# Kernel optimization log

Measured on AMD Instinct MI355X. Metric: run time of the kernel, lower is better.

## Reference

```python
import jax, jax.numpy as jnp
import numpy as np

HEAD_DIM = 32
KERNEL = 3
DILATION = 2


def _unfold(x, k, dil):
    """torch.nn.Unfold with stride=1, padding=dil*(k-1)//2.
    x: [B, C, H, W] -> patches [B, C, k*k, H, W] (kernel positions row-major,
    channel-major overall, matching torch's (B, C*k*k, L) layout)."""
    B, C, H, W = x.shape
    pad = dil * (k - 1) // 2
    xp = jnp.pad(x, ((0, 0), (0, 0), (pad, pad), (pad, pad)))
    patches = jnp.stack(
        [xp[:, :, i * dil:i * dil + H, j * dil:j * dil + W]
         for i in range(k) for j in range(k)],
        axis=2,
    )
    return patches  # [B, C, k*k, H, W]


def setup_inputs() -> dict:
    key = jax.random.key(0)
    kq, kk, kv = jax.random.split(key, 3)
    shape = (8, 384, 56, 56)
    return {
        "q": jax.random.normal(kq, shape, dtype=jnp.float32),
        "k": jax.random.normal(kk, shape, dtype=jnp.float32),
        "v": jax.random.normal(kv, shape, dtype=jnp.float32),
    }


def reference(q, k, v):
    B, d, H, W = q.shape
    h = d // HEAD_DIM
    N = H * W
    k2 = KERNEL * KERNEL
    scale = HEAD_DIM ** (-0.5)

    # q: [B, h, N, hd]
    qr = q.reshape(B, h, HEAD_DIM, N).transpose(0, 1, 3, 2)
    # k patches: [B, h, hd, k2, N]
    kp = _unfold(k, KERNEL, DILATION).reshape(B, h, HEAD_DIM, k2, N)
    attn = jnp.einsum('bhnd,bhdkn->bhnk', qr, kp) * scale
    attn = jax.nn.softmax(attn, axis=-1)
    # v patches: [B, h, hd, k2, N]
    vp = _unfold(v, KERNEL, DILATION).reshape(B, h, HEAD_DIM, k2, N)
    out = jnp.einsum('bhnk,bhdkn->bhnd', attn, vp)  # [B, h, N, hd]
    # transpose(1,2) then reshape(B, H, W, d)
    return out.transpose(0, 2, 1, 3).reshape(B, H, W, d)
```

## Files before the change

kernel.cpp:

```cpp
#include <hip/hip_runtime.h>

#define HD 32
#define NHEADS 12
#define HH 56
#define WW 56
#define NN (HH * WW)
#define BB 8
#define CC (HD * NHEADS)

__global__ __launch_bounds__(256) void dilate_attn_kernel(
    const float* __restrict__ q,
    const float* __restrict__ k,
    const float* __restrict__ v,
    float* __restrict__ out)
{
    const int n = blockIdx.x * blockDim.x + threadIdx.x;
    if (n >= NN) return;
    const int bh = blockIdx.y;
    const int b = bh / NHEADS;
    const int head = bh - b * NHEADS;
    const int y = n / WW;
    const int x = n - y * WW;

    const size_t base = ((size_t)b * CC + (size_t)head * HD) * NN;
    const float* qb = q + base + n;

    float qv[HD];
#pragma unroll
    for (int d = 0; d < HD; ++d) qv[d] = qb[(size_t)d * NN];

    float lg[9];
#pragma unroll
    for (int kk = 0; kk < 9; ++kk) {
        const int dy = ((kk / 3) - 1) * 2;
        const int dx = ((kk % 3) - 1) * 2;
        const int ny = y + dy;
        const int nx = x + dx;
        float s = 0.f;
        if ((unsigned)ny < HH && (unsigned)nx < WW) {
            const float* kb = k + base + (size_t)(ny * WW + nx);
#pragma unroll
            for (int d = 0; d < HD; ++d) s = fmaf(qv[d], kb[(size_t)d * NN], s);
        }
        lg[kk] = s * 0.17677669529663689f;
    }

    float m = lg[0];
#pragma unroll
    for (int kk = 1; kk < 9; ++kk) m = fmaxf(m, lg[kk]);
    float wsum = 0.f;
#pragma unroll
    for (int kk = 0; kk < 9; ++kk) { lg[kk] = __expf(lg[kk] - m); wsum += lg[kk]; }
    const float inv = 1.f / wsum;

    float acc[HD];
#pragma unroll
    for (int d = 0; d < HD; ++d) acc[d] = 0.f;
#pragma unroll
    for (int kk = 0; kk < 9; ++kk) {
        const int dy = ((kk / 3) - 1) * 2;
        const int dx = ((kk % 3) - 1) * 2;
        const int ny = y + dy;
        const int nx = x + dx;
        if ((unsigned)ny < HH && (unsigned)nx < WW) {
            const float w = lg[kk] * inv;
            const float* vb = v + base + (size_t)(ny * WW + nx);
#pragma unroll
            for (int d = 0; d < HD; ++d) acc[d] = fmaf(w, vb[(size_t)d * NN], acc[d]);
        }
    }

    float* ob = out + (((size_t)b * HH + y) * WW + x) * CC + (size_t)head * HD;
#pragma unroll
    for (int d = 0; d < HD; d += 4) {
        float4 val = make_float4(acc[d], acc[d + 1], acc[d + 2], acc[d + 3]);
        *reinterpret_cast<float4*>(ob + d) = val;
    }
}

extern "C" void kernel_launch(void* const* d_in, const int* in_sizes, int n_in,
                              void* d_out, int out_size, void* d_ws, size_t ws_size,
                              hipStream_t stream) {
    const float* q = (const float*)d_in[0];
    const float* k = (const float*)d_in[1];
    const float* v = (const float*)d_in[2];
    float* out = (float*)d_out;

    dim3 block(256);
    dim3 grid((NN + 255) / 256, BB * NHEADS);
    dilate_attn_kernel<<<grid, block, 0, stream>>>(q, k, v, out);
}
```

Measured before the change: 188.8 us.

## Split head dimension across two thread halves with shared-memory logit reduction

Result: no change. 185.2 us (-1.9%).

```diff
diff --git a/kernel.cpp b/kernel.cpp
--- a/kernel.cpp
+++ b/kernel.cpp
@@ -1,12 +1,15 @@
 #include <hip/hip_runtime.h>
 
 #define HD 32
+#define HALF 16
 #define NHEADS 12
 #define HH 56
 #define WW 56
 #define NN (HH * WW)
 #define BB 8
 #define CC (HD * NHEADS)
+#define TILE_N 128
+#define SCALE 0.17677669529663689f
 
 __global__ __launch_bounds__(256) void dilate_attn_kernel(
     const float* __restrict__ q,
@@ -14,67 +17,85 @@
     const float* __restrict__ v,
     float* __restrict__ out)
 {
-    const int n = blockIdx.x * blockDim.x + threadIdx.x;
-    if (n >= NN) return;
+    const int xi = threadIdx.x;
+    const int half = threadIdx.y;
+    const int n = blockIdx.x * TILE_N + xi;
     const int bh = blockIdx.y;
     const int b = bh / NHEADS;
     const int head = bh - b * NHEADS;
+    const bool active = (n < NN);
+
     const int y = n / WW;
     const int x = n - y * WW;
 
-    const size_t base = ((size_t)b * CC + (size_t)head * HD) * NN;
-    const float* qb = q + base + n;
+    const size_t base = ((size_t)b * CC + (size_t)head * HD + (size_t)half * HALF) * NN;
 
-    float qv[HD];
+    __shared__ float part[2][TILE_N][9];
+
+    float qv[HALF];
+    if (active) {
+        const float* qb = q + base + n;
 #pragma unroll
-    for (int d = 0; d < HD; ++d) qv[d] = qb[(size_t)d * NN];
+        for (int d = 0; d < HALF; ++d) qv[d] = qb[(size_t)d * NN];
+    }
 
     float lg[9];
 #pragma unroll
-    for (int kk = 0; kk < 9; ++kk) {
-        const int dy = ((kk / 3) - 1) * 2;
-        const int dx = ((kk % 3) - 1) * 2;
+    for (int t = 0; t < 9; ++t) {
+        const int dy = ((t / 3) - 1) * 2;
+        const int dx = ((t % 3) - 1) * 2;
         const int ny = y + dy;
         const int nx = x + dx;
         float s = 0.f;
-        if ((unsigned)ny < HH && (unsigned)nx < WW) {
+        if (active && (unsigned)ny < HH && (unsigned)nx < WW) {
             const float* kb = k + base + (size_t)(ny * WW + nx);
 #pragma unroll
-            for (int d = 0; d < HD; ++d) s = fmaf(qv[d], kb[(size_t)d * NN], s);
+            for (int d = 0; d < HALF; ++d) s = fmaf(qv[d], kb[(size_t)d * NN], s);
         }
-        lg[kk] = s * 0.17677669529663689f;
+        lg[t] = s;
+        part[half][xi][t] = s;
     }
+    __syncthreads();
 
+    {
+        const int other = 1 - half;
+#pragma unroll
+        for (int t = 0; t < 9; ++t)
+            lg[t] = (lg[t] + part[other][xi][t]) * SCALE;
+    }
     float m = lg[0];
 #pragma unroll
-    for (int kk = 1; kk < 9; ++kk) m = fmaxf(m, lg[kk]);
+    for (int t = 1; t < 9; ++t) m = fmaxf(m, lg[t]);
     float wsum = 0.f;
 #pragma unroll
-    for (int kk = 0; kk < 9; ++kk) { lg[kk] = __expf(lg[kk] - m); wsum += lg[kk]; }
+    for (int t = 0; t < 9; ++t) { lg[t] = __expf(lg[t] - m); wsum += lg[t]; }
     const float inv = 1.f / wsum;
 
-    float acc[HD];
+    float acc[HALF];
 #pragma unroll
-    for (int d = 0; d < HD; ++d) acc[d] = 0.f;
+    for (int d = 0; d < HALF; ++d) acc[d] = 0.f;
 #pragma unroll
-    for (int kk = 0; kk < 9; ++kk) {
-        const int dy = ((kk / 3) - 1) * 2;
-        const int dx = ((kk % 3) - 1) * 2;
+    for (int t = 0; t < 9; ++t) {
+        const int dy = ((t / 3) - 1) * 2;
+        const int dx = ((t % 3) - 1) * 2;
         const int ny = y + dy;
         const int nx = x + dx;
-        if ((unsigned)ny < HH && (unsigned)nx < WW) {
-            const float w = lg[kk] * inv;
+        if (active && (unsigned)ny < HH && (unsigned)nx < WW) {
+            const float w = lg[t] * inv;
             const float* vb = v + base + (size_t)(ny * WW + nx);
 #pragma unroll
-            for (int d = 0; d < HD; ++d) acc[d] = fmaf(w, vb[(size_t)d * NN], acc[d]);
+            for (int d = 0; d < HALF; ++d) acc[d] = fmaf(w, vb[(size_t)d * NN], acc[d]);
         }
     }
 
-    float* ob = out + (((size_t)b * HH + y) * WW + x) * CC + (size_t)head * HD;
+    if (active) {
+        float* ob = out + (((size_t)b * HH + y) * WW + x) * CC
+                    + (size_t)head * HD + (size_t)half * HALF;
 #pragma unroll
-    for (int d = 0; d < HD; d += 4) {
-        float4 val = make_float4(acc[d], acc[d + 1], acc[d + 2], acc[d + 3]);
-        *reinterpret_cast<float4*>(ob + d) = val;
+        for (int d = 0; d < HALF; d += 4) {
+            float4 val = make_float4(acc[d], acc[d + 1], acc[d + 2], acc[d + 3]);
+            *reinterpret_cast<float4*>(ob + d) = val;
+        }
     }
 }
 
@@ -86,7 +107,7 @@
     const float* v = (const float*)d_in[2];
     float* out = (float*)d_out;
 
-    dim3 block(256);
-    dim3 grid((NN + 255) / 256, BB * NHEADS);
+    dim3 block(TILE_N, 2);
+    dim3 grid((NN + TILE_N - 1) / TILE_N, BB * NHEADS);
     dilate_attn_kernel<<<grid, block, 0, stream>>>(q, k, v, out);
 }
```
